# Kernel optimization log

Hardware: AMD Instinct MI355X
Metric: run time of the kernel (lower is better)

Reference implementation:

```python
import jax, jax.numpy as jnp
import numpy as np

N_HEADS = 16
N_KV_HEADS = 4
HEAD_DIM = 64
ROPE_BASE = 10000.0

def _rope_cos_sin(T, dtype):
    # flash-attn style: cos/sin of shape [T, head_dim//2]
    inv_freq = 1.0 / (ROPE_BASE ** (jnp.arange(0, HEAD_DIM, 2, dtype=jnp.float32) / HEAD_DIM))
    freqs = jnp.arange(T, dtype=jnp.float32)[:, None] * inv_freq[None, :]  # [T, D/2]
    return jnp.cos(freqs).astype(dtype), jnp.sin(freqs).astype(dtype)

def _apply_rope(x, cos, sin):
    # x: [B, H, T, D], non-interleaved rotate-half on full head dim
    d2 = HEAD_DIM // 2
    x1, x2 = x[..., :d2], x[..., d2:]
    c = cos[None, None, :, :]
    s = sin[None, None, :, :]
    return jnp.concatenate([x1 * c - x2 * s, x2 * c + x1 * s], axis=-1)

def setup_inputs() -> dict:
    key = jax.random.key(0)
    ks = jax.random.split(key, 6)
    B, T, D = 1, 4096, 1024
    def g(k, shape, scale):
        return jax.random.normal(k, shape, dtype=jnp.float32) * scale
    return {
        "query": g(ks[0], (B, T, D), 1.0),
        "Wq": g(ks[1], (D, D), D ** -0.5),
        "Wk": g(ks[2], (D, N_KV_HEADS * HEAD_DIM), D ** -0.5),
        "Wv": g(ks[3], (D, N_KV_HEADS * HEAD_DIM), D ** -0.5),
        "W1": g(ks[4], (D, 4 * D), D ** -0.5),
        "W2": g(ks[5], (4 * D, D), (4 * D) ** -0.5),
    }

def reference(query, Wq, Wk, Wv, W1, W2):
    B, T, D = query.shape
    # QKV projections -> [B, H, T, Dh]
    q = (query @ Wq).reshape(B, T, N_HEADS, HEAD_DIM).transpose(0, 2, 1, 3)
    k = (query @ Wk).reshape(B, T, N_KV_HEADS, HEAD_DIM).transpose(0, 2, 1, 3)
    v = (query @ Wv).reshape(B, T, N_KV_HEADS, HEAD_DIM).transpose(0, 2, 1, 3)
    # RoPE (seqlen_offset = 0, no cache)
    cos, sin = _rope_cos_sin(T, q.dtype)
    q = _apply_rope(q, cos, sin)
    k = _apply_rope(k, cos, sin)
    # GQA: repeat KV heads to match Q heads
    n_rep = N_HEADS // N_KV_HEADS
    k = jnp.repeat(k, n_rep, axis=1)
    v = jnp.repeat(v, n_rep, axis=1)
    # Scaled dot-product attention, causal
    scale = HEAD_DIM ** -0.5
    scores = jnp.einsum("bhqd,bhkd->bhqk", q, k) * scale
    i = jnp.arange(T)[:, None]
    j = jnp.arange(T)[None, :]
    scores = jnp.where(j > i, jnp.finfo(scores.dtype).min, scores)
    attn = jax.nn.softmax(scores, axis=-1)
    out = jnp.einsum("bhqk,bhkd->bhqd", attn, v)  # [B, H, T, Dh]
    out = out.transpose(0, 2, 1, 3).reshape(B, T, D)
    # out_proj: Linear -> SiLU -> Linear (use_swiglu=True path)
    return jax.nn.silu(out @ W1) @ W2
```

## Files before the change

### kernel.cpp

```cpp
#include <hip/hip_runtime.h>
#include <stdint.h>

typedef unsigned short u16;
typedef __bf16 bf16x8 __attribute__((ext_vector_type(8)));
typedef float f32x4 __attribute__((ext_vector_type(4)));

#define T_SEQ 4096
#define DMODEL 1024

__device__ __forceinline__ float bf2f(u16 x) {
  union { uint32_t u; float f; } v; v.u = ((uint32_t)x) << 16; return v.f;
}
__device__ __forceinline__ u16 f2bf(float f) {
  union { float f; uint32_t u; } v; v.f = f;
  return (u16)((v.u + 0x7FFFu + ((v.u >> 16) & 1u)) >> 16);
}
__device__ __forceinline__ float fexp2(float x) {
#if __has_builtin(__builtin_amdgcn_exp2f)
  return __builtin_amdgcn_exp2f(x);
#else
  return __expf(x * 0.6931471805599453f);
#endif
}
__device__ __forceinline__ uint32_t asu32(float f) {
  union { float f; uint32_t u; } v; v.f = f; return v.u;
}
__device__ __forceinline__ uint32_t bfpack(uint32_t hi, uint32_t lo) {
  return __builtin_amdgcn_perm(hi, lo, 0x07060302u);
}
__device__ __forceinline__ void async16(void* lds, const void* g) {
  __builtin_amdgcn_global_load_lds(
      (__attribute__((address_space(1))) void*)const_cast<void*>(g),
      (__attribute__((address_space(3))) void*)lds, 16, 0, 0);
}
__device__ __forceinline__ void storeC(u16* C, size_t i, float v) { C[i] = f2bf(v); }
__device__ __forceinline__ void storeC(float* C, size_t i, float v) { C[i] = v; }

__global__ void __launch_bounds__(256) f2b_copy(const float* __restrict__ in,
                                                u16* __restrict__ out, int n) {
  int idx = (blockIdx.x * 256 + threadIdx.x) * 4;
  if (idx >= n) return;
  float4 v = *(const float4*)(in + idx);
  union { u16 s[4]; uint2 q; } b;
  b.s[0] = f2bf(v.x); b.s[1] = f2bf(v.y); b.s[2] = f2bf(v.z); b.s[3] = f2bf(v.w);
  *(uint2*)(out + idx) = b.q;
}

__global__ void __launch_bounds__(256) wtrans(const float* __restrict__ in,
                                              u16* __restrict__ out, int K, int N) {
  __shared__ float tile[64][65];
  const int n0 = blockIdx.x * 64, k0 = blockIdx.y * 64;
  const int tid = threadIdx.x;
  const int r = tid >> 2, c = (tid & 3) * 16;
#pragma unroll
  for (int j = 0; j < 4; ++j) {
    float4 v = *(const float4*)&in[(size_t)(k0 + r) * N + n0 + c + j * 4];
    tile[r][c + j * 4 + 0] = v.x; tile[r][c + j * 4 + 1] = v.y;
    tile[r][c + j * 4 + 2] = v.z; tile[r][c + j * 4 + 3] = v.w;
  }
  __syncthreads();
  union { u16 s[16]; uint4 q[2]; } buf;
#pragma unroll
  for (int j = 0; j < 16; ++j) buf.s[j] = f2bf(tile[c + j][r]);
  u16* dst = out + (size_t)(n0 + r) * K + k0 + c;
  *(uint4*)(dst) = buf.q[0];
  *(uint4*)(dst + 8) = buf.q[1];
}

__global__ void __launch_bounds__(256) vtrans(const u16* __restrict__ qkv,
                                              u16* __restrict__ Vt) {
  __shared__ u16 tile[64][65];
  const int t0 = blockIdx.x * 64, h = blockIdx.y;
  const int tid = threadIdx.x;
  const int r = tid >> 2, q4 = (tid & 3) * 16;
  const u16* src = qkv + (size_t)(t0 + r) * 1536 + 1280 + h * 64 + q4;
  union { u16 s[16]; uint4 q[2]; } buf;
  buf.q[0] = *(const uint4*)(src);
  buf.q[1] = *(const uint4*)(src + 8);
#pragma unroll
  for (int j = 0; j < 16; ++j) tile[r][q4 + j] = buf.s[j];
  __syncthreads();
#pragma unroll
  for (int j = 0; j < 16; ++j) buf.s[j] = tile[q4 + j][r];
  u16* dst = Vt + ((size_t)h * 64 + r) * T_SEQ + t0 + q4;
  *(uint4*)(dst) = buf.q[0];
  *(uint4*)(dst + 8) = buf.q[1];
}

__global__ void __launch_bounds__(256) rope_qk(const u16* __restrict__ qkv,
                                               u16* __restrict__ Q, u16* __restrict__ Ko) {
  const int t = blockIdx.x;
  const int tid = threadIdx.x;
  const int i = tid & 31;
  const float ang = (float)t * powf(10000.f, -(float)i * (1.f / 32.f));
  float s, c;
  sincosf(ang, &s, &c);
  const u16* row = qkv + (size_t)t * 1536;
  const float QS = 0.125f * 1.4426950408889634f;
  const float cq = c * QS, sq = s * QS;
#pragma unroll
  for (int it = 0; it < 2; ++it) {
    int h = (tid >> 5) + it * 8;
    float x1 = bf2f(row[h * 64 + i]);
    float x2 = bf2f(row[h * 64 + 32 + i]);
    size_t o = ((size_t)h * T_SEQ + t) * 64 + i;
    Q[o] = f2bf(x1 * cq - x2 * sq);
    Q[o + 32] = f2bf(x2 * cq + x1 * sq);
  }
  if (tid < 128) {
    int h = tid >> 5;
    float x1 = bf2f(row[1024 + h * 64 + i]);
    float x2 = bf2f(row[1024 + h * 64 + 32 + i]);
    size_t o = ((size_t)h * T_SEQ + t) * 64 + i;
    Ko[o] = f2bf(x1 * c - x2 * s);
    Ko[o + 32] = f2bf(x2 * c + x1 * s);
  }
}

template <int AM, int ACT, typename OutT>
__global__ void __launch_bounds__(256) gemm_bt(const u16* __restrict__ A,
                                               const u16* __restrict__ Bt,
                                               OutT* __restrict__ C,
                                               int M, int N, int K) {
  __shared__ u16 sA[AM * 32][64];
  __shared__ u16 sB[128][64];
  const int tid = threadIdx.x;
  const int w = tid >> 6, lane = tid & 63;
  const int g = lane >> 4, l15 = lane & 15;
  const int r8 = lane >> 3, c8 = lane & 7;
  const int bm = blockIdx.y * (AM * 32), bn = blockIdx.x * 128;

  f32x4 acc[AM][4];
#pragma unroll
  for (int i = 0; i < AM; ++i)
#pragma unroll
    for (int j = 0; j < 4; ++j) acc[i][j] = (f32x4){0.f, 0.f, 0.f, 0.f};

  const u16* Ag = A + (size_t)(bm + w * (AM * 8) + r8) * K + (c8 ^ r8) * 8;
  const u16* Bg = Bt + (size_t)(bn + w * 32 + r8) * K + (c8 ^ r8) * 8;
  const int mrow = (w >> 1) * (AM * 16), ncol = (w & 1) * 64;
  const int swz = l15 & 7;

  for (int k0 = 0; k0 < K; k0 += 64) {
#pragma unroll
    for (int t = 0; t < AM; ++t)
      async16(&sA[w * (AM * 8) + t * 8][0], Ag + (size_t)(t * 8) * K + k0);
#pragma unroll
    for (int t = 0; t < 4; ++t)
      async16(&sB[w * 32 + t * 8][0], Bg + (size_t)(t * 8) * K + k0);
    __syncthreads();
#pragma unroll
    for (int kk = 0; kk < 2; ++kk) {
      const int cb = ((kk * 4 + g) ^ swz) * 8;
      bf16x8 a[AM], b[4];
#pragma unroll
      for (int i = 0; i < AM; ++i) a[i] = *(const bf16x8*)&sA[mrow + i * 16 + l15][cb];
#pragma unroll
      for (int i = 0; i < 4; ++i) b[i] = *(const bf16x8*)&sB[ncol + i * 16 + l15][cb];
#pragma unroll
      for (int mi = 0; mi < AM; ++mi)
#pragma unroll
        for (int ni = 0; ni < 4; ++ni)
          acc[mi][ni] = __builtin_amdgcn_mfma_f32_16x16x32_bf16(a[mi], b[ni], acc[mi][ni], 0, 0, 0);
    }
    __syncthreads();
  }
#pragma unroll
  for (int mi = 0; mi < AM; ++mi)
#pragma unroll
    for (int ni = 0; ni < 4; ++ni)
#pragma unroll
      for (int r = 0; r < 4; ++r) {
        int row = bm + mrow + mi * 16 + g * 4 + r;
        int col = bn + ncol + ni * 16 + l15;
        float v = acc[mi][ni][r];
        if (ACT == 1) v = v / (1.f + __expf(-v));
        storeC(C, (size_t)row * N + col, v);
      }
}

__global__ void __launch_bounds__(256) attn(const u16* __restrict__ Q,
                                            const u16* __restrict__ K,
                                            const u16* __restrict__ Vt,
                                            u16* __restrict__ O) {
  __shared__ u16 sK[2][64][64];
  __shared__ u16 sV[2][64][64];
  __shared__ u16 sP[4][32][72];
  const int pr = blockIdx.x;
  const int h = blockIdx.y;
  const int kvh = h >> 2;
  const int tid = threadIdx.x;
  const int w = tid >> 6, lane = tid & 63;
  const int g = lane >> 4, l15 = lane & 15;
  const int r8 = lane >> 3, c8 = lane & 7;
  const int swz = l15 & 7;
  const int t0 = pr, t1 = 63 - pr;
  const int thr = w * 16 + l15;

  bf16x8 qf[2][2];
  {
    const u16* Qh = Q + (size_t)h * T_SEQ * 64;
#pragma unroll
    for (int half = 0; half < 2; ++half) {
      const int q = (half ? t1 : t0) * 64 + w * 16 + l15;
#pragma unroll
      for (int kk = 0; kk < 2; ++kk)
        qf[half][kk] = *(const bf16x8*)(Qh + (size_t)q * 64 + (kk * 4 + g) * 8);
    }
  }

  float lsum[2] = {0.f, 0.f};
  f32x4 oacc[2][4];
#pragma unroll
  for (int half = 0; half < 2; ++half)
#pragma unroll
    for (int nd = 0; nd < 4; ++nd) oacc[half][nd] = (f32x4){0.f, 0.f, 0.f, 0.f};

  const u16* Kg = K + ((size_t)kvh * T_SEQ + w * 16 + r8) * 64 + (c8 ^ r8) * 8;
  const u16* Vg = Vt + ((size_t)kvh * 64 + w * 16 + r8) * T_SEQ + (c8 ^ r8) * 8;

#define STAGE(J, B)                                                     \
  {                                                                     \
    const int kv0_ = (J) * 64;                                          \
    async16(&sK[B][w * 16 + 0][0], Kg + (size_t)kv0_ * 64);             \
    async16(&sK[B][w * 16 + 8][0], Kg + (size_t)(kv0_ + 8) * 64);       \
    async16(&sV[B][w * 16 + 0][0], Vg + kv0_);                          \
    async16(&sV[B][w * 16 + 8][0], Vg + (size_t)8 * T_SEQ + kv0_);      \
  }

#define BODY(B, BOTH, MASK0, MASK1)                                               \
  {                                                                               \
    const int b_ = (B);                                                           \
    f32x4 s0[4], s1[4];                                                           \
    _Pragma("unroll") for (int kt = 0; kt < 4; ++kt) {                            \
      s1[kt] = (f32x4){0.f, 0.f, 0.f, 0.f};                                       \
      if (BOTH) s0[kt] = (f32x4){0.f, 0.f, 0.f, 0.f};                             \
    }                                                                             \
    _Pragma("unroll") for (int kt = 0; kt < 4; ++kt)                              \
    _Pragma("unroll") for (int kk = 0; kk < 2; ++kk) {                            \
      bf16x8 kf = *(const bf16x8*)&sK[b_][kt * 16 + l15][((kk * 4 + g) ^ swz) * 8]; \
      s1[kt] = __builtin_amdgcn_mfma_f32_16x16x32_bf16(kf, qf[1][kk], s1[kt], 0, 0, 0); \
      if (BOTH)                                                                   \
        s0[kt] = __builtin_amdgcn_mfma_f32_16x16x32_bf16(kf, qf[0][kk], s0[kt], 0, 0, 0); \
    }                                                                             \
    _Pragma("unroll") for (int kt = 0; kt < 4; ++kt) {                            \
      uint32_t u_[4];                                                             \
      _Pragma("unroll") for (int r = 0; r < 4; ++r) {                             \
        float p = fexp2(s1[kt][r]);                                               \
        if (MASK1 && (kt * 16 + g * 4 + r > thr)) p = 0.f;                        \
        lsum[1] += p;                                                             \
        u_[r] = asu32(p) + 0x8000u;                                               \
      }                                                                           \
      uint2 pk;                                                                   \
      pk.x = bfpack(u_[1], u_[0]);                                                \
      pk.y = bfpack(u_[3], u_[2]);                                                \
      *(uint2*)&sP[w][16 + l15][kt * 16 + g * 4] = pk;                            \
    }                                                                             \
    if (BOTH) {                                                                   \
      _Pragma("unroll") for (int kt = 0; kt < 4; ++kt) {                          \
        uint32_t u_[4];                                                           \
        _Pragma("unroll") for (int r = 0; r < 4; ++r) {                           \
          float p = fexp2(s0[kt][r]);                                             \
          if (MASK0 && (kt * 16 + g * 4 + r > thr)) p = 0.f;                      \
          lsum[0] += p;                                                           \
          u_[r] = asu32(p) + 0x8000u;                                             \
        }                                                                         \
        uint2 pk;                                                                 \
        pk.x = bfpack(u_[1], u_[0]);                                              \
        pk.y = bfpack(u_[3], u_[2]);                                              \
        *(uint2*)&sP[w][l15][kt * 16 + g * 4] = pk;                               \
      }                                                                           \
    }                                                                             \
    __builtin_amdgcn_wave_barrier();       \
    _Pragma("unroll") for (int kk = 0; kk < 2; ++kk) {                            \
      bf16x8 pf1 = *(const bf16x8*)&sP[w][16 + l15][kk * 32 + g * 8];             \
      bf16x8 pf0;                                                                 \
      if (BOTH) pf0 = *(const bf16x8*)&sP[w][l15][kk * 32 + g * 8];               \
      _Pragma("unroll") for (int nd = 0; nd < 4; ++nd) {                          \
        bf16x8 vf = *(const bf16x8*)&sV[b_][nd * 16 + l15][((kk * 4 + g) ^ swz) * 8]; \
        oacc[1][nd] = __builtin_amdgcn_mfma_f32_16x16x32_bf16(pf1, vf, oacc[1][nd], 0, 0, 0); \
        if (BOTH)                                                                 \
          oacc[0][nd] = __builtin_amdgcn_mfma_f32_16x16x32_bf16(pf0, vf, oacc[0][nd], 0, 0, 0); \
      }                                                                           \
    }                                                                             \
  }

  STAGE(0, 0);
  int j = 0;
  for (; j < t0; ++j) {
    __syncthreads();
    STAGE(j + 1, (j + 1) & 1);
    BODY(j & 1, true, false, false);
  }
  {
    __syncthreads();
    STAGE(j + 1, (j + 1) & 1);
    BODY(j & 1, true, true, false);
    ++j;
  }
  for (; j < t1; ++j) {
    __syncthreads();
    STAGE(j + 1, (j + 1) & 1);
    BODY(j & 1, false, false, false);
  }
  {
    __syncthreads();
    BODY(j & 1, false, false, true);
  }
#undef STAGE
#undef BODY

#pragma unroll
  for (int half = 0; half < 2; ++half) {
    const int q0 = (half ? t1 : t0) * 64;
    float l = lsum[half];
    l += __shfl_xor(l, 16);
    l += __shfl_xor(l, 32);
#pragma unroll
    for (int r = 0; r < 4; ++r) {
      const float inv = 1.f / __shfl(l, g * 4 + r, 16);
      const int trow = q0 + w * 16 + g * 4 + r;
#pragma unroll
      for (int nd = 0; nd < 4; ++nd)
        O[(size_t)trow * DMODEL + h * 64 + nd * 16 + l15] = f2bf(oacc[half][nd][r] * inv);
    }
  }
}

extern "C" void kernel_launch(void* const* d_in, const int* in_sizes, int n_in,
                              void* d_out, int out_size, void* d_ws, size_t ws_size,
                              hipStream_t stream) {
  const float* query = (const float*)d_in[0];
  const float* Wq = (const float*)d_in[1];
  const float* Wk = (const float*)d_in[2];
  const float* Wv = (const float*)d_in[3];
  const float* W1 = (const float*)d_in[4];
  const float* W2 = (const float*)d_in[5];
  float* out = (float*)d_out;

  char* ws = (char*)d_ws;
  size_t off = 0;
  auto alloc = [&](size_t bytes) { char* p = ws + off; off += (bytes + 255) & ~(size_t)255; return p; };
  u16* Xb   = (u16*)alloc((size_t)4096 * 1024 * 2);
  u16* QKVb = (u16*)alloc((size_t)4096 * 1536 * 2);
  u16* Qb   = (u16*)alloc((size_t)16 * 4096 * 64 * 2);
  u16* Kb   = (u16*)alloc((size_t)4 * 4096 * 64 * 2);
  u16* Vtb  = (u16*)alloc((size_t)4 * 4096 * 64 * 2);
  u16* H    = (u16*)ws;
  u16* WqkvT = (u16*)alloc((size_t)1536 * 1024 * 2);
  u16* W1T   = (u16*)alloc((size_t)4096 * 1024 * 2);
  u16* W2T   = (u16*)alloc((size_t)1024 * 4096 * 2);
  u16* AO    = (u16*)alloc((size_t)4096 * 1024 * 2);
  (void)ws_size; (void)in_sizes; (void)n_in; (void)out_size;

  f2b_copy<<<4096, 256, 0, stream>>>(query, Xb, 4096 * 1024);
  wtrans<<<dim3(16, 16), 256, 0, stream>>>(Wq, WqkvT, 1024, 1024);
  wtrans<<<dim3(4, 16), 256, 0, stream>>>(Wk, WqkvT + (size_t)1024 * 1024, 1024, 256);
  wtrans<<<dim3(4, 16), 256, 0, stream>>>(Wv, WqkvT + (size_t)1280 * 1024, 1024, 256);
  wtrans<<<dim3(64, 16), 256, 0, stream>>>(W1, W1T, 1024, 4096);
  wtrans<<<dim3(16, 64), 256, 0, stream>>>(W2, W2T, 4096, 1024);

  gemm_bt<2, 0, u16><<<dim3(12, 64), 256, 0, stream>>>(Xb, WqkvT, QKVb, 4096, 1536, 1024);
  rope_qk<<<4096, 256, 0, stream>>>(QKVb, Qb, Kb);
  vtrans<<<dim3(64, 4), 256, 0, stream>>>(QKVb, Vtb);
  attn<<<dim3(32, 16), 256, 0, stream>>>(Qb, Kb, Vtb, AO);
  gemm_bt<4, 1, u16><<<dim3(32, 32), 256, 0, stream>>>(AO, W1T, H, 4096, 4096, 1024);
  gemm_bt<2, 0, float><<<dim3(8, 64), 256, 0, stream>>>(H, W2T, out, 4096, 1024, 4096);
}
```

Before: 321.6 us.

## Enlarge attention query tile to 128 rows and compute row sums via MFMA

The attention kernel now processes 128-query tiles per half (each wave handles 32 rows as two 16-row sub-tiles), so each staged K/V tile is reused across twice as many queries and the grid is halved to 16x16 blocks. Softmax row sums come from an MFMA against a ones vector instead of scalar adds and shuffles. Bf16 packing uses the hardware cvt_pk_bf16 instruction when available, and the P buffer is XOR-swizzled to cut LDS bank conflicts. The cost is more registers (launch bounds set to 1 block), fewer blocks than CUs on the device, and extra masked diagonal iterations.

```diff
diff --git a/kernel.cpp b/kernel.cpp
--- a/kernel.cpp
+++ b/kernel.cpp
@@ -22,11 +22,17 @@
   return __expf(x * 0.6931471805599453f);
 #endif
 }
-__device__ __forceinline__ uint32_t asu32(float f) {
-  union { float f; uint32_t u; } v; v.f = f; return v.u;
-}
-__device__ __forceinline__ uint32_t bfpack(uint32_t hi, uint32_t lo) {
-  return __builtin_amdgcn_perm(hi, lo, 0x07060302u);
+__device__ __forceinline__ uint32_t pack_bf16(float lo, float hi) {
+#if __has_builtin(__builtin_amdgcn_cvt_pk_bf16_f32)
+  typedef __bf16 bf16x2_t __attribute__((ext_vector_type(2)));
+  union { bf16x2_t v; uint32_t u; } c;
+  c.v = __builtin_amdgcn_cvt_pk_bf16_f32(lo, hi);
+  return c.u;
+#else
+  union { float f; uint32_t u; } a, b;
+  a.f = lo; b.f = hi;
+  return __builtin_amdgcn_perm(b.u + 0x8000u, a.u + 0x8000u, 0x07060302u);
+#endif
 }
 __device__ __forceinline__ void async16(void* lds, const void* g) {
   __builtin_amdgcn_global_load_lds(
@@ -179,13 +185,13 @@
       }
 }
 
-__global__ void __launch_bounds__(256) attn(const u16* __restrict__ Q,
-                                            const u16* __restrict__ K,
-                                            const u16* __restrict__ Vt,
-                                            u16* __restrict__ O) {
+__global__ void __launch_bounds__(256, 1) attn(const u16* __restrict__ Q,
+                                               const u16* __restrict__ K,
+                                               const u16* __restrict__ Vt,
+                                               u16* __restrict__ O) {
   __shared__ u16 sK[2][64][64];
   __shared__ u16 sV[2][64][64];
-  __shared__ u16 sP[4][32][72];
+  __shared__ u16 sP[4][64][64];
   const int pr = blockIdx.x;
   const int h = blockIdx.y;
   const int kvh = h >> 2;
@@ -193,28 +199,41 @@
   const int w = tid >> 6, lane = tid & 63;
   const int g = lane >> 4, l15 = lane & 15;
   const int r8 = lane >> 3, c8 = lane & 7;
-  const int swz = l15 & 7;
-  const int t0 = pr, t1 = 63 - pr;
-  const int thr = w * 16 + l15;
-
-  bf16x8 qf[2][2];
+  const int swz = l15 & 7, d3 = l15 & 3;
+  const int t0 = pr, t1 = 31 - pr;
+
+  bf16x8 qf[2][2][2];
   {
     const u16* Qh = Q + (size_t)h * T_SEQ * 64;
 #pragma unroll
-    for (int half = 0; half < 2; ++half) {
-      const int q = (half ? t1 : t0) * 64 + w * 16 + l15;
-#pragma unroll
-      for (int kk = 0; kk < 2; ++kk)
-        qf[half][kk] = *(const bf16x8*)(Qh + (size_t)q * 64 + (kk * 4 + g) * 8);
+    for (int half = 0; half < 2; ++half)
+#pragma unroll
+      for (int mi = 0; mi < 2; ++mi) {
+        const int q = (half ? t1 : t0) * 128 + w * 32 + mi * 16 + l15;
+#pragma unroll
+        for (int kk = 0; kk < 2; ++kk)
+          qf[half][mi][kk] = *(const bf16x8*)(Qh + (size_t)q * 64 + (kk * 4 + g) * 8);
+      }
+  }
+
+  f32x4 oacc[2][2][4];
+  f32x4 lacc[2][2];
+#pragma unroll
+  for (int half = 0; half < 2; ++half)
+#pragma unroll
+    for (int mi = 0; mi < 2; ++mi) {
+      lacc[half][mi] = (f32x4){0.f, 0.f, 0.f, 0.f};
+#pragma unroll
+      for (int nd = 0; nd < 4; ++nd) oacc[half][mi][nd] = (f32x4){0.f, 0.f, 0.f, 0.f};
     }
-  }
-
-  float lsum[2] = {0.f, 0.f};
-  f32x4 oacc[2][4];
-#pragma unroll
-  for (int half = 0; half < 2; ++half)
-#pragma unroll
-    for (int nd = 0; nd < 4; ++nd) oacc[half][nd] = (f32x4){0.f, 0.f, 0.f, 0.f};
+
+  bf16x8 ONES;
+  {
+    union { u16 s[8]; bf16x8 v; } o;
+#pragma unroll
+    for (int i = 0; i < 8; ++i) o.s[i] = 0x3F80;
+    ONES = o.v;
+  }
 
   const u16* Kg = K + ((size_t)kvh * T_SEQ + w * 16 + r8) * 64 + (c8 ^ r8) * 8;
   const u16* Vg = Vt + ((size_t)kvh * 64 + w * 16 + r8) * T_SEQ + (c8 ^ r8) * 8;
@@ -228,102 +247,127 @@
     async16(&sV[B][w * 16 + 8][0], Vg + (size_t)8 * T_SEQ + kv0_);      \
   }
 
-#define BODY(B, BOTH, MASK0, MASK1)                                               \
+#define BODY(B, ACT0, M0, M1, OFF)                                                \
   {                                                                               \
     const int b_ = (B);                                                           \
-    f32x4 s0[4], s1[4];                                                           \
+    f32x4 s1[2][4], s0[2][4];                                                     \
+    _Pragma("unroll") for (int mi = 0; mi < 2; ++mi)                              \
     _Pragma("unroll") for (int kt = 0; kt < 4; ++kt) {                            \
-      s1[kt] = (f32x4){0.f, 0.f, 0.f, 0.f};                                       \
-      if (BOTH) s0[kt] = (f32x4){0.f, 0.f, 0.f, 0.f};                             \
+      s1[mi][kt] = (f32x4){0.f, 0.f, 0.f, 0.f};                                   \
+      if (ACT0) s0[mi][kt] = (f32x4){0.f, 0.f, 0.f, 0.f};                         \
     }                                                                             \
     _Pragma("unroll") for (int kt = 0; kt < 4; ++kt)                              \
     _Pragma("unroll") for (int kk = 0; kk < 2; ++kk) {                            \
       bf16x8 kf = *(const bf16x8*)&sK[b_][kt * 16 + l15][((kk * 4 + g) ^ swz) * 8]; \
-      s1[kt] = __builtin_amdgcn_mfma_f32_16x16x32_bf16(kf, qf[1][kk], s1[kt], 0, 0, 0); \
-      if (BOTH)                                                                   \
-        s0[kt] = __builtin_amdgcn_mfma_f32_16x16x32_bf16(kf, qf[0][kk], s0[kt], 0, 0, 0); \
+      _Pragma("unroll") for (int mi = 0; mi < 2; ++mi) {                          \
+        s1[mi][kt] = __builtin_amdgcn_mfma_f32_16x16x32_bf16(kf, qf[1][mi][kk], s1[mi][kt], 0, 0, 0); \
+        if (ACT0)                                                                 \
+          s0[mi][kt] = __builtin_amdgcn_mfma_f32_16x16x32_bf16(kf, qf[0][mi][kk], s0[mi][kt], 0, 0, 0); \
+      }                                                                           \
     }                                                                             \
-    _Pragma("unroll") for (int kt = 0; kt < 4; ++kt) {                            \
-      uint32_t u_[4];                                                             \
-      _Pragma("unroll") for (int r = 0; r < 4; ++r) {                             \
-        float p = fexp2(s1[kt][r]);                                               \
-        if (MASK1 && (kt * 16 + g * 4 + r > thr)) p = 0.f;                        \
-        lsum[1] += p;                                                             \
-        u_[r] = asu32(p) + 0x8000u;                                               \
-      }                                                                           \
-      uint2 pk;                                                                   \
-      pk.x = bfpack(u_[1], u_[0]);                                                \
-      pk.y = bfpack(u_[3], u_[2]);                                                \
-      *(uint2*)&sP[w][16 + l15][kt * 16 + g * 4] = pk;                            \
-    }                                                                             \
-    if (BOTH) {                                                                   \
+    _Pragma("unroll") for (int mi = 0; mi < 2; ++mi) {                            \
+      const int thr_ = w * 32 + mi * 16 + l15 - (OFF);                            \
       _Pragma("unroll") for (int kt = 0; kt < 4; ++kt) {                          \
-        uint32_t u_[4];                                                           \
+        float p_[4];                                                              \
         _Pragma("unroll") for (int r = 0; r < 4; ++r) {                           \
-          float p = fexp2(s0[kt][r]);                                             \
-          if (MASK0 && (kt * 16 + g * 4 + r > thr)) p = 0.f;                      \
-          lsum[0] += p;                                                           \
-          u_[r] = asu32(p) + 0x8000u;                                             \
+          float p = fexp2(s1[mi][kt][r]);                                         \
+          if (M1 && (kt * 16 + g * 4 + r > thr_)) p = 0.f;                        \
+          p_[r] = p;                                                              \
         }                                                                         \
         uint2 pk;                                                                 \
-        pk.x = bfpack(u_[1], u_[0]);                                              \
-        pk.y = bfpack(u_[3], u_[2]);                                              \
-        *(uint2*)&sP[w][l15][kt * 16 + g * 4] = pk;                               \
+        pk.x = pack_bf16(p_[0], p_[1]);                                           \
+        pk.y = pack_bf16(p_[2], p_[3]);                                           \
+        *(uint2*)&sP[w][32 + mi * 16 + l15][(kt ^ d3) * 16 + g * 4] = pk;         \
+      }                                                                           \
+      if (ACT0) {                                                                 \
+        _Pragma("unroll") for (int kt = 0; kt < 4; ++kt) {                        \
+          float p_[4];                                                            \
+          _Pragma("unroll") for (int r = 0; r < 4; ++r) {                         \
+            float p = fexp2(s0[mi][kt][r]);                                       \
+            if (M0 && (kt * 16 + g * 4 + r > thr_)) p = 0.f;                      \
+            p_[r] = p;                                                            \
+          }                                                                       \
+          uint2 pk;                                                               \
+          pk.x = pack_bf16(p_[0], p_[1]);                                         \
+          pk.y = pack_bf16(p_[2], p_[3]);                                         \
+          *(uint2*)&sP[w][mi * 16 + l15][(kt ^ d3) * 16 + g * 4] = pk;            \
+        }                                                                         \
       }                                                                           \
     }                                                                             \
-    __builtin_amdgcn_wave_barrier();       \
+    __builtin_amdgcn_wave_barrier();          \
     _Pragma("unroll") for (int kk = 0; kk < 2; ++kk) {                            \
-      bf16x8 pf1 = *(const bf16x8*)&sP[w][16 + l15][kk * 32 + g * 8];             \
-      bf16x8 pf0;                                                                 \
-      if (BOTH) pf0 = *(const bf16x8*)&sP[w][l15][kk * 32 + g * 8];               \
+      const int pb_ = (((kk * 2 + (g >> 1)) ^ d3) * 16 + (g & 1) * 8);            \
+      bf16x8 pf1[2], pf0[2];                                                      \
+      _Pragma("unroll") for (int mi = 0; mi < 2; ++mi) {                          \
+        pf1[mi] = *(const bf16x8*)&sP[w][32 + mi * 16 + l15][pb_];                \
+        if (ACT0) pf0[mi] = *(const bf16x8*)&sP[w][mi * 16 + l15][pb_];           \
+      }                                                                           \
+      _Pragma("unroll") for (int mi = 0; mi < 2; ++mi) {                          \
+        lacc[1][mi] = __builtin_amdgcn_mfma_f32_16x16x32_bf16(pf1[mi], ONES, lacc[1][mi], 0, 0, 0); \
+        if (ACT0)                                                                 \
+          lacc[0][mi] = __builtin_amdgcn_mfma_f32_16x16x32_bf16(pf0[mi], ONES, lacc[0][mi], 0, 0, 0); \
+      }                                                                           \
       _Pragma("unroll") for (int nd = 0; nd < 4; ++nd) {                          \
         bf16x8 vf = *(const bf16x8*)&sV[b_][nd * 16 + l15][((kk * 4 + g) ^ swz) * 8]; \
-        oacc[1][nd] = __builtin_amdgcn_mfma_f32_16x16x32_bf16(pf1, vf, oacc[1][nd], 0, 0, 0); \
-        if (BOTH)                                                                 \
-          oacc[0][nd] = __builtin_amdgcn_mfma_f32_16x16x32_bf16(pf0, vf, oacc[0][nd], 0, 0, 0); \
+        _Pragma("unroll") for (int mi = 0; mi < 2; ++mi) {                        \
+          oacc[1][mi][nd] = __builtin_amdgcn_mfma_f32_16x16x32_bf16(pf1[mi], vf, oacc[1][mi][nd], 0, 0, 0); \
+          if (ACT0)                                                               \
+            oacc[0][mi][nd] = __builtin_amdgcn_mfma_f32_16x16x32_bf16(pf0[mi], vf, oacc[0][mi][nd], 0, 0, 0); \
+        }                                                                         \
       }                                                                           \
     }                                                                             \
   }
 
   STAGE(0, 0);
   int j = 0;
-  for (; j < t0; ++j) {
+  for (; j < 2 * t0; ++j) {
     __syncthreads();
     STAGE(j + 1, (j + 1) & 1);
-    BODY(j & 1, true, false, false);
+    BODY(j & 1, true, false, false, 0);
   }
   {
     __syncthreads();
     STAGE(j + 1, (j + 1) & 1);
-    BODY(j & 1, true, true, false);
+    BODY(j & 1, true, true, false, 0);
     ++j;
   }
-  for (; j < t1; ++j) {
+  {
     __syncthreads();
     STAGE(j + 1, (j + 1) & 1);
-    BODY(j & 1, false, false, false);
-  }
-  {
-    __syncthreads();
-    BODY(j & 1, false, false, true);
+    BODY(j & 1, true, true, false, 64);
+    ++j;
+  }
+  for (; j < 2 * t1; ++j) {
+    __syncthreads();
+    STAGE(j + 1, (j + 1) & 1);
+    BODY(j & 1, false, false, false, 0);
+  }
+  {
+    __syncthreads();
+    STAGE(j + 1, (j + 1) & 1);
+    BODY(j & 1, false, false, true, 0);
+    ++j;
+  }
+  {
+    __syncthreads();
+    BODY(j & 1, false, false, true, 64);
   }
 #undef STAGE
 #undef BODY
 
 #pragma unroll
   for (int half = 0; half < 2; ++half) {
-    const int q0 = (half ? t1 : t0) * 64;
-    float l = lsum[half];
-    l += __shfl_xor(l, 16);
-    l += __shfl_xor(l, 32);
-#pragma unroll
-    for (int r = 0; r < 4; ++r) {
-      const float inv = 1.f / __shfl(l, g * 4 + r, 16);
-      const int trow = q0 + w * 16 + g * 4 + r;
-#pragma unroll
-      for (int nd = 0; nd < 4; ++nd)
-        O[(size_t)trow * DMODEL + h * 64 + nd * 16 + l15] = f2bf(oacc[half][nd][r] * inv);
-    }
+    const int tb = (half ? t1 : t0) * 128;
+#pragma unroll
+    for (int mi = 0; mi < 2; ++mi)
+#pragma unroll
+      for (int r = 0; r < 4; ++r) {
+        const float inv = 1.f / lacc[half][mi][r];
+        const int trow = tb + w * 32 + mi * 16 + g * 4 + r;
+#pragma unroll
+        for (int nd = 0; nd < 4; ++nd)
+          O[(size_t)trow * DMODEL + h * 64 + nd * 16 + l15] = f2bf(oacc[half][mi][nd][r] * inv);
+      }
   }
 }
 
@@ -363,7 +407,7 @@
   gemm_bt<2, 0, u16><<<dim3(12, 64), 256, 0, stream>>>(Xb, WqkvT, QKVb, 4096, 1536, 1024);
   rope_qk<<<4096, 256, 0, stream>>>(QKVb, Qb, Kb);
   vtrans<<<dim3(64, 4), 256, 0, stream>>>(QKVb, Vtb);
-  attn<<<dim3(32, 16), 256, 0, stream>>>(Qb, Kb, Vtb, AO);
+  attn<<<dim3(16, 16), 256, 0, stream>>>(Qb, Kb, Vtb, AO);
   gemm_bt<4, 1, u16><<<dim3(32, 32), 256, 0, stream>>>(AO, W1T, H, 4096, 4096, 1024);
   gemm_bt<2, 0, float><<<dim3(8, 64), 256, 0, stream>>>(H, W2T, out, 4096, 1024, 4096);
 }
```

New measurement: 344.5 us. 1.07x slower.
